# Kernel tuning notes

Measured on AMD Instinct MI355X. Metric: run time of the kernel, lower is better.

## Reference

```python
import jax, jax.numpy as jnp
import numpy as np


def setup_inputs() -> dict:
    key = jax.random.key(0)
    k1, k2, k3, k4 = jax.random.split(key, 4)
    B, S, IN, OUT, K = 4, 2048, 4096, 4096, 256
    x = jax.random.normal(k1, (B, S, IN), dtype=jnp.float32)
    centroids = jax.random.normal(k2, (K,), dtype=jnp.float32)
    bias = jax.random.normal(k3, (OUT,), dtype=jnp.float32)
    indices = jax.random.randint(k4, (OUT, IN), 0, K, dtype=jnp.int64)
    return {"x": x, "centroids": centroids, "bias": bias, "indices": indices}


def reference(x, centroids, bias, indices):
    # Reconstruct the weight matrix from the codebook: [out, in]
    weight = centroids[indices]
    # F.linear: y = x @ weight.T + bias
    out = jnp.einsum('bsi,oi->bso', x, weight) + bias
    return out
```

## Files before the change

kernel.cpp:

```cpp
#include <hip/hip_runtime.h>
#include <hip/hip_bf16.h>
#include <stdint.h>


typedef unsigned short u16;
typedef __attribute__((ext_vector_type(8))) short short8;
typedef __attribute__((ext_vector_type(8))) u16   u16x8;
typedef __attribute__((ext_vector_type(4))) float f32x4;
typedef __attribute__((ext_vector_type(4))) int   i32x4;

constexpr int Mdim = 8192;
constexpr int Ndim = 4096;
constexpr int Kdim = 4096;

__device__ __forceinline__ u16 f2bf(float f) {
  union { float f; uint32_t u; } v; v.f = f;
  uint32_t u = v.u;
  return (u16)((u + 0x7fffu + ((u >> 16) & 1u)) >> 16);
}

__global__ void decode_weight_kernel(const int* __restrict__ idx,
                                     const float* __restrict__ cent,
                                     u16* __restrict__ wb) {
  __shared__ u16 lut[256];
  const int t = threadIdx.x;
  if (t < 256) lut[t] = f2bf(cent[t]);
  __syncthreads();
  const size_t base = ((size_t)blockIdx.x * 256 + t) * 8;
  i32x4 i0 = *(const i32x4*)(idx + base);
  i32x4 i1 = *(const i32x4*)(idx + base + 4);
  u16x8 r;
  r[0] = lut[i0[0] & 255]; r[1] = lut[i0[1] & 255];
  r[2] = lut[i0[2] & 255]; r[3] = lut[i0[3] & 255];
  r[4] = lut[i1[0] & 255]; r[5] = lut[i1[1] & 255];
  r[6] = lut[i1[2] & 255]; r[7] = lut[i1[3] & 255];
  *(u16x8*)(wb + base) = r;
}

__global__ void cvt_x_kernel(const float* __restrict__ x, u16* __restrict__ xb) {
  const size_t base = ((size_t)blockIdx.x * 256 + threadIdx.x) * 8;
  f32x4 a = *(const f32x4*)(x + base);
  f32x4 b = *(const f32x4*)(x + base + 4);
  u16x8 r;
  r[0] = f2bf(a[0]); r[1] = f2bf(a[1]); r[2] = f2bf(a[2]); r[3] = f2bf(a[3]);
  r[4] = f2bf(b[0]); r[5] = f2bf(b[1]); r[6] = f2bf(b[2]); r[7] = f2bf(b[3]);
  *(u16x8*)(xb + base) = r;
}

__device__ __forceinline__ void async16(const u16* g, u16* l) {
  __builtin_amdgcn_global_load_lds(
      (const __attribute__((address_space(1))) void*)g,
      (__attribute__((address_space(3))) void*)l,
      16, 0, 0);
}

#define BAR()   __builtin_amdgcn_s_barrier()
#define LGKM0() asm volatile("s_waitcnt lgkmcnt(0)" ::: "memory")
#define LGKM4() asm volatile("s_waitcnt lgkmcnt(4)" ::: "memory")
#define VMC4()  asm volatile("s_waitcnt vmcnt(4)" ::: "memory")
#define VMC0()  asm volatile("s_waitcnt vmcnt(0)" ::: "memory")

__global__ __launch_bounds__(512, 2)
void gemm_bf16_kernel(const u16* __restrict__ A,
                      const u16* __restrict__ B,
                      const float* __restrict__ bias,
                      float* __restrict__ C) {
  __shared__ u16 AsF[32768];
  __shared__ u16 BsF[32768];

  const int t    = threadIdx.x;
  const int lane = t & 63;
  const int w    = t >> 6;
  const int wm   = w >> 2;
  const int wn   = w & 3;
  const int fr   = lane & 15;
  const int fq   = lane >> 4;
  const int cswz = (fr & 6) << 2;

  const int bid = blockIdx.x;
  const int swz = (bid & 7) * 64 + (bid >> 3);
  const int m0 = (swz >> 4) * 256;
  const int n0 = (swz & 15) * 256;

  const int c0   = w * 64 + lane;
  const int r16s = (c0 & 63) >> 2;
  const int srow = ((c0 >> 7) << 4) + r16s;
  const int scol = ((c0 >> 6) & 1) * 32 + (((c0 & 3) * 8) ^ ((r16s & 6) << 2));
  const u16* pA = A + (size_t)(m0 + srow) * Kdim + scol;
  const u16* pB = B + (size_t)(n0 + srow) * Kdim + scol;
  const int dsto = c0 * 8;

  const int aoff = wm * 8192 + fr * 32 + ((fq * 8) ^ cswz);
  const int boff = (wn >> 1) * 8192 + (wn & 1) * 4096 + fr * 32 + ((fq * 8) ^ cswz);

  f32x4 acc[8][4] = {};
  short8 bf[2][4];
  short8 afA[2][2];
  short8 afB[2][2];

  auto stageA = [&](int tk, int h) {
    const u16* s = pA + (size_t)h * (128 * Kdim) + tk * 64;
    u16* d = &AsF[((tk & 1) * 2 + h) * 8192 + dsto];
    async16(s, d);
    async16(s + (size_t)(64 * Kdim), d + 4096);
  };
  auto stageB = [&](int tk, int h) {
    const u16* s = pB + (size_t)h * (128 * Kdim) + tk * 64;
    u16* d = &BsF[((tk & 1) * 2 + h) * 8192 + dsto];
    async16(s, d);
    async16(s + (size_t)(64 * Kdim), d + 4096);
  };
  auto rdB_kk = [&](int BUF, int kk) {
#pragma unroll
    for (int ni = 0; ni < 4; ++ni)
      bf[kk][ni] = *(const short8*)&BsF[BUF * 16384 + boff + (ni * 2 + kk) * 512];
  };
  auto rdA_A = [&](int BUF, int q) {
#pragma unroll
    for (int kk = 0; kk < 2; ++kk)
#pragma unroll
      for (int i = 0; i < 2; ++i)
        afA[kk][i] = *(const short8*)&AsF[BUF * 16384 + aoff + ((q * 2 + i) * 2 + kk) * 512];
  };
  auto rdA_B = [&](int BUF, int q) {
#pragma unroll
    for (int kk = 0; kk < 2; ++kk)
#pragma unroll
      for (int i = 0; i < 2; ++i)
        afB[kk][i] = *(const short8*)&AsF[BUF * 16384 + aoff + ((q * 2 + i) * 2 + kk) * 512];
  };
  auto mfmaE = [&](int q) {
    __builtin_amdgcn_s_setprio(1);
#pragma unroll
    for (int kk = 0; kk < 2; ++kk)
#pragma unroll
      for (int i = 0; i < 2; ++i)
#pragma unroll
        for (int ni = 0; ni < 4; ++ni)
          acc[q * 2 + i][ni] = __builtin_amdgcn_mfma_f32_16x16x32_bf16(
              afA[kk][i], bf[kk][ni], acc[q * 2 + i][ni], 0, 0, 0);
    __builtin_amdgcn_s_setprio(0);
  };
  auto mfmaO = [&](int q) {
    __builtin_amdgcn_s_setprio(1);
#pragma unroll
    for (int kk = 0; kk < 2; ++kk)
#pragma unroll
      for (int i = 0; i < 2; ++i)
#pragma unroll
        for (int ni = 0; ni < 4; ++ni)
          acc[q * 2 + i][ni] = __builtin_amdgcn_mfma_f32_16x16x32_bf16(
              afB[kk][i], bf[kk][ni], acc[q * 2 + i][ni], 0, 0, 0);
    __builtin_amdgcn_s_setprio(0);
  };
  auto mfmaO_kk = [&](int q, int kk) {
    __builtin_amdgcn_s_setprio(1);
#pragma unroll
    for (int i = 0; i < 2; ++i)
#pragma unroll
      for (int ni = 0; ni < 4; ++ni)
        acc[q * 2 + i][ni] = __builtin_amdgcn_mfma_f32_16x16x32_bf16(
            afB[kk][i], bf[kk][ni], acc[q * 2 + i][ni], 0, 0, 0);
    __builtin_amdgcn_s_setprio(0);
  };

#define KT(TK, BUF, DOA, DOB, MODE)                                     \
  {                                                                     \
                                                                \
    rdA_B((BUF), 1);                                                    \
    if (DOA) stageA((TK) + 1, 0);                                       \
    BAR(); LGKM4();            \
    mfmaE(0);                                                           \
    BAR();                                                              \
                                                                \
    rdA_A((BUF), 2);                                                    \
    if (DOA) stageA((TK) + 1, 1);                                       \
    if (DOB) stageB((TK) + 2, 0);                                       \
    BAR(); LGKM4();                                   \
    mfmaO(1);                                                           \
    BAR();                                                              \
                                                                \
    rdA_B((BUF), 3);                                                    \
    if (DOB) stageB((TK) + 2, 1);                                       \
    BAR(); LGKM4();                                   \
    mfmaE(2);                                                           \
    BAR();                                                              \
                                                      \
    if ((MODE) == 0) { VMC4(); } else if ((MODE) == 1) { VMC0(); }      \
    BAR();                         \
    LGKM0();                                          \
    mfmaO_kk(3, 0);                                                     \
    if ((MODE) < 2) rdB_kk((BUF) ^ 1, 0);                               \
    mfmaO_kk(3, 1);                                                     \
    if ((MODE) < 2) { rdB_kk((BUF) ^ 1, 1); rdA_A((BUF) ^ 1, 0); }      \
    BAR();                                                              \
  }

  stageA(0, 0); stageA(0, 1); stageB(0, 0); stageB(0, 1);
  stageB(1, 0); stageB(1, 1);
  VMC4();
  BAR();
  rdB_kk(0, 0); rdB_kk(0, 1); rdA_A(0, 0);

  for (int t2 = 0; t2 < 31; ++t2) {
    const int k0 = 2 * t2;
    KT(k0,     0, 1, 1, 0);
    KT(k0 + 1, 1, 1, 1, 0);
  }
  KT(62, 0, 1, 0, 1);
  KT(63, 1, 0, 0, 2);

  float bv[4];
#pragma unroll
  for (int ni = 0; ni < 4; ++ni)
    bv[ni] = bias[n0 + wn * 64 + ni * 16 + fr];

#pragma unroll
  for (int mi = 0; mi < 8; ++mi) {
#pragma unroll
    for (int j = 0; j < 4; ++j) {
      const int row = m0 + wm * 128 + mi * 16 + fq * 4 + j;
      float* cp = C + (size_t)row * Ndim + n0 + wn * 64 + fr;
#pragma unroll
      for (int ni = 0; ni < 4; ++ni)
        cp[ni * 16] = acc[mi][ni][j] + bv[ni];
    }
  }
#undef KT
}

extern "C" void kernel_launch(void* const* d_in, const int* in_sizes, int n_in,
                              void* d_out, int out_size, void* d_ws, size_t ws_size,
                              hipStream_t stream) {
  const float* x    = (const float*)d_in[0];
  const float* cent = (const float*)d_in[1];
  const float* bias = (const float*)d_in[2];
  const int*   idx  = (const int*)d_in[3];
  float* out = (float*)d_out;

  u16* wb = (u16*)d_ws;
  u16* xb = (u16*)((char*)d_ws + (size_t)Ndim * Kdim * sizeof(u16));

  decode_weight_kernel<<<(Ndim * Kdim) / (256 * 8), 256, 0, stream>>>(idx, cent, wb);
  cvt_x_kernel<<<((size_t)Mdim * Kdim) / (256 * 8), 256, 0, stream>>>(x, xb);

  gemm_bf16_kernel<<<dim3(512), 512, 0, stream>>>(xb, wb, bias, out);
}
```

Before: 285.0 us.

## Triple-buffer A tiles in LDS and prefetch two K-steps ahead

```diff
diff --git a/kernel.cpp b/kernel.cpp
--- a/kernel.cpp
+++ b/kernel.cpp
@@ -55,9 +55,10 @@
 }
 
 #define BAR()   __builtin_amdgcn_s_barrier()
-#define LGKM0() asm volatile("s_waitcnt lgkmcnt(0)" ::: "memory")
-#define LGKM4() asm volatile("s_waitcnt lgkmcnt(4)" ::: "memory")
-#define VMC4()  asm volatile("s_waitcnt vmcnt(4)" ::: "memory")
+#define SCB()   __builtin_amdgcn_sched_barrier(0)
+#define LGKM0() do { asm volatile("s_waitcnt lgkmcnt(0)" ::: "memory"); SCB(); } while (0)
+#define LGKM4() do { asm volatile("s_waitcnt lgkmcnt(4)" ::: "memory"); SCB(); } while (0)
+#define VMC8()  asm volatile("s_waitcnt vmcnt(8)" ::: "memory")
 #define VMC0()  asm volatile("s_waitcnt vmcnt(0)" ::: "memory")
 
 __global__ __launch_bounds__(512, 2)
@@ -65,7 +66,7 @@
                       const u16* __restrict__ B,
                       const float* __restrict__ bias,
                       float* __restrict__ C) {
-  __shared__ u16 AsF[32768];
+  __shared__ u16 AsF[49152];
   __shared__ u16 BsF[32768];
 
   const int t    = threadIdx.x;
@@ -98,36 +99,36 @@
   short8 afA[2][2];
   short8 afB[2][2];
 
-  auto stageA = [&](int tk, int h) {
+  auto stageA = [&](int tk, int h, int buf) {
     const u16* s = pA + (size_t)h * (128 * Kdim) + tk * 64;
-    u16* d = &AsF[((tk & 1) * 2 + h) * 8192 + dsto];
+    u16* d = &AsF[buf * 16384 + h * 8192 + dsto];
     async16(s, d);
     async16(s + (size_t)(64 * Kdim), d + 4096);
   };
-  auto stageB = [&](int tk, int h) {
+  auto stageB = [&](int tk, int h, int buf) {
     const u16* s = pB + (size_t)h * (128 * Kdim) + tk * 64;
-    u16* d = &BsF[((tk & 1) * 2 + h) * 8192 + dsto];
+    u16* d = &BsF[buf * 16384 + h * 8192 + dsto];
     async16(s, d);
     async16(s + (size_t)(64 * Kdim), d + 4096);
   };
-  auto rdB_kk = [&](int BUF, int kk) {
+  auto rdB_kk = [&](int buf, int kk) {
 #pragma unroll
     for (int ni = 0; ni < 4; ++ni)
-      bf[kk][ni] = *(const short8*)&BsF[BUF * 16384 + boff + (ni * 2 + kk) * 512];
-  };
-  auto rdA_A = [&](int BUF, int q) {
-#pragma unroll
-    for (int kk = 0; kk < 2; ++kk)
-#pragma unroll
-      for (int i = 0; i < 2; ++i)
-        afA[kk][i] = *(const short8*)&AsF[BUF * 16384 + aoff + ((q * 2 + i) * 2 + kk) * 512];
-  };
-  auto rdA_B = [&](int BUF, int q) {
-#pragma unroll
-    for (int kk = 0; kk < 2; ++kk)
-#pragma unroll
-      for (int i = 0; i < 2; ++i)
-        afB[kk][i] = *(const short8*)&AsF[BUF * 16384 + aoff + ((q * 2 + i) * 2 + kk) * 512];
+      bf[kk][ni] = *(const short8*)&BsF[buf * 16384 + boff + (ni * 2 + kk) * 512];
+  };
+  auto rdA_A = [&](int buf, int q) {
+#pragma unroll
+    for (int kk = 0; kk < 2; ++kk)
+#pragma unroll
+      for (int i = 0; i < 2; ++i)
+        afA[kk][i] = *(const short8*)&AsF[buf * 16384 + aoff + ((q * 2 + i) * 2 + kk) * 512];
+  };
+  auto rdA_B = [&](int buf, int q) {
+#pragma unroll
+    for (int kk = 0; kk < 2; ++kk)
+#pragma unroll
+      for (int i = 0; i < 2; ++i)
+        afB[kk][i] = *(const short8*)&AsF[buf * 16384 + aoff + ((q * 2 + i) * 2 + kk) * 512];
   };
   auto mfmaE = [&](int q) {
     __builtin_amdgcn_s_setprio(1);
@@ -164,51 +165,48 @@
     __builtin_amdgcn_s_setprio(0);
   };
 
-#define KT(TK, BUF, DOA, DOB, MODE)                                     \
-  {                                                                     \
-                                                                \
-    rdA_B((BUF), 1);                                                    \
-    if (DOA) stageA((TK) + 1, 0);                                       \
-    BAR(); LGKM4();            \
-    mfmaE(0);                                                           \
-    BAR();                                                              \
-                                                                \
-    rdA_A((BUF), 2);                                                    \
-    if (DOA) stageA((TK) + 1, 1);                                       \
-    if (DOB) stageB((TK) + 2, 0);                                       \
-    BAR(); LGKM4();                                   \
-    mfmaO(1);                                                           \
-    BAR();                                                              \
-                                                                \
-    rdA_B((BUF), 3);                                                    \
-    if (DOB) stageB((TK) + 2, 1);                                       \
-    BAR(); LGKM4();                                   \
-    mfmaE(2);                                                           \
-    BAR();                                                              \
-                                                      \
-    if ((MODE) == 0) { VMC4(); } else if ((MODE) == 1) { VMC0(); }      \
-    BAR();                         \
-    LGKM0();                                          \
-    mfmaO_kk(3, 0);                                                     \
-    if ((MODE) < 2) rdB_kk((BUF) ^ 1, 0);                               \
-    mfmaO_kk(3, 1);                                                     \
-    if ((MODE) < 2) { rdB_kk((BUF) ^ 1, 1); rdA_A((BUF) ^ 1, 0); }      \
-    BAR();                                                              \
-  }
-
-  stageA(0, 0); stageA(0, 1); stageB(0, 0); stageB(0, 1);
-  stageB(1, 0); stageB(1, 1);
-  VMC4();
+  auto tile = [&](int tk, int ab, int bb, int mode) {
+    const int abN = (ab == 2) ? 0 : ab + 1;
+    const int ab2 = (abN == 2) ? 0 : abN + 1;
+    rdA_B(ab, 1);
+    if (mode == 0) stageA(tk + 2, 0, ab2);
+    BAR(); LGKM4();
+    mfmaE(0);
+    BAR();
+    rdA_A(ab, 2);
+    if (mode == 0) stageA(tk + 2, 1, ab2);
+    BAR(); LGKM4();
+    mfmaO(1);
+    BAR();
+    rdA_B(ab, 3);
+    if (mode == 0) stageB(tk + 2, 0, bb);
+    BAR(); LGKM4();
+    mfmaE(2);
+    BAR();
+    if (mode == 0) { stageB(tk + 2, 1, bb); VMC8(); }
+    else if (mode == 1) { VMC0(); }
+    BAR();
+    LGKM0();
+    mfmaO_kk(3, 0);
+    if (mode < 2) rdB_kk(bb ^ 1, 0);
+    mfmaO_kk(3, 1);
+    if (mode < 2) { rdB_kk(bb ^ 1, 1); rdA_A(abN, 0); }
+    BAR();
+  };
+
+  stageA(0, 0, 0); stageA(0, 1, 0); stageB(0, 0, 0); stageB(0, 1, 0);
+  stageA(1, 0, 1); stageA(1, 1, 1); stageB(1, 0, 1); stageB(1, 1, 1);
+  VMC8();
   BAR();
   rdB_kk(0, 0); rdB_kk(0, 1); rdA_A(0, 0);
 
-  for (int t2 = 0; t2 < 31; ++t2) {
-    const int k0 = 2 * t2;
-    KT(k0,     0, 1, 1, 0);
-    KT(k0 + 1, 1, 1, 1, 0);
+  int ab = 0;
+  for (int tk = 0; tk < 62; ++tk) {
+    tile(tk, ab, tk & 1, 0);
+    ab = (ab == 2) ? 0 : ab + 1;
   }
-  KT(62, 0, 1, 0, 1);
-  KT(63, 1, 0, 0, 2);
+  tile(62, 2, 0, 1);
+  tile(63, 0, 1, 2);
 
   float bv[4];
 #pragma unroll
@@ -226,7 +224,6 @@
         cp[ni * 16] = acc[mi][ni][j] + bv[ni];
     }
   }
-#undef KT
 }
 
 extern "C" void kernel_launch(void* const* d_in, const int* in_sizes, int n_in,
```

Result: slower. 333.9 us (+17.1%).
